# Kernel optimization log

Hardware: AMD Instinct MI355X
Metric: run time of the kernel (lower is better)

## Reference

```python
import jax, jax.numpy as jnp
from jax import lax
import numpy as np

# db4 filter bank (pywt convention): rec_lo is the canonical Daubechies-4 scaling filter
_REC_LO = np.array([0.23037781330885523, 0.7148465705525415, 0.6308807679295904,
                    -0.02798376941698385, -0.18703481171888114, 0.030841381835986965,
                    0.032883011666982945, -0.010597401784997278])
L = 8
_DEC_LO = _REC_LO[::-1].copy()
_DEC_HI = _REC_LO * ((-1.0) ** (np.arange(L) + 1))  # pywt dec_hi
_REC_HI = _DEC_HI[::-1].copy()
LEVEL = 2


def dwt_step(x):
    """Single-level DWT, pywt 'symmetric' mode. x: (N, S) -> a, d: (N, floor((S+L-1)/2))."""
    n, s = x.shape
    ext = jnp.pad(x, ((0, 0), (L - 1, L - 1)), mode='symmetric')[:, 1:]  # start at conv index 1
    # XLA conv is correlation; flip dec filters to get true convolution
    k = jnp.stack([_DEC_LO[::-1], _DEC_HI[::-1]]).astype(x.dtype)[:, None, :]  # (2,1,L)
    y = lax.conv_general_dilated(ext[:, None, :], k, window_strides=(2,), padding='VALID',
                                 dimension_numbers=('NCH', 'OIH', 'NCH'))  # (N,2,Lc)
    return y[:, 0], y[:, 1]


def idwt_step(a, d):
    """Single-level inverse DWT (pywt). Output length 2*la - L + 2."""
    la = a.shape[1]
    coef = jnp.stack([a, d], axis=1)  # (N,2,la)
    k = jnp.stack([_REC_LO[::-1], _REC_HI[::-1]]).astype(a.dtype)[None, :, :]  # (1,2,L) summed over a/d
    y = lax.conv_general_dilated(coef, k, window_strides=(1,), padding=[(L - 1, L - 1)],
                                 lhs_dilation=(2,),  # upsample-by-2 then full convolution
                                 dimension_numbers=('NCH', 'OIH', 'NCH'))  # (N,1,2la+L-2)
    return y[:, 0, L - 2: L - 2 + (2 * la - L + 2)]


def soft(c, t):
    return jnp.sign(c) * jnp.maximum(jnp.abs(c) - t, 0.0)


def denoise_2d(x2d):
    """x2d: (N, S) batch of signals; wavedec->soft-threshold->waverec, per-signal threshold."""
    s = x2d.shape[1]
    a = x2d
    details = []  # appended finest-first: [d1, d2]
    for _ in range(LEVEL):
        a, d = dwt_step(a)
        details.append(d)
    d1 = details[0]  # coeffs[-1] in pywt ordering = finest detail
    sigma = jnp.median(jnp.abs(d1), axis=1) / 0.6745
    thr = (sigma * jnp.sqrt(2.0 * jnp.log(jnp.asarray(s, x2d.dtype))))[:, None]
    rec = soft(a, thr)
    for d in details[::-1]:  # coarsest-first reconstruction
        d = soft(d, thr)
        rec = rec[:, : d.shape[1]]  # pywt waverec crops approx when one longer than detail
        rec = idwt_step(rec, d)
    return rec[:, :s]


def setup_inputs() -> dict:
    key = jax.random.key(0)
    x = jax.random.normal(key, (32, 8192, 64), dtype=jnp.float32)
    return {"x": x}


def reference(x):
    b, s, f = x.shape
    x2 = jnp.transpose(x, (0, 2, 1)).reshape(b * f, s)  # (B*F, S): every signal independent
    y = denoise_2d(x2)
    return y.reshape(b, f, s).transpose(0, 2, 1)
```

## Files before the change

kernel.cpp:

```cpp
#include <hip/hip_runtime.h>

#define S0LEN 8192
#define L1LEN 4099
#define L2LEN 2053
#define NROWS 2048
#define NT    256
#define NT2   512

constexpr float DEC_LO[8] = {
  -0.010597401784997278f,  0.032883011666982945f,  0.030841381835986965f,
  -0.18703481171888114f,  -0.02798376941698385f,   0.6308807679295904f,
   0.7148465705525415f,    0.23037781330885523f };
constexpr float DEC_HI[8] = {
  -0.23037781330885523f,   0.7148465705525415f,   -0.6308807679295904f,
  -0.02798376941698385f,   0.18703481171888114f,   0.030841381835986965f,
  -0.032883011666982945f, -0.010597401784997278f };
constexpr float REC_LO[8] = {
   0.23037781330885523f,   0.7148465705525415f,    0.6308807679295904f,
  -0.02798376941698385f,  -0.18703481171888114f,   0.030841381835986965f,
   0.032883011666982945f, -0.010597401784997278f };
constexpr float REC_HI[8] = {
  -0.010597401784997278f, -0.032883011666982945f,  0.030841381835986965f,
   0.18703481171888114f,  -0.02798376941698385f,  -0.6308807679295904f,
   0.7148465705525415f,   -0.23037781330885523f };

__device__ __forceinline__ int refl(int m, int n) {
  m = (m < 0) ? (-1 - m) : m;
  m = (m >= n) ? (2 * n - 1 - m) : m;
  return m;
}

__device__ __forceinline__ float softf(float c, float t) {
  float m = fmaxf(fabsf(c) - t, 0.0f);
  return copysignf(m, c);
}

__device__ __forceinline__ void dwt_stage(const float* __restrict__ src, int n_in,
                                          float* __restrict__ outA,
                                          float* __restrict__ outD,
                                          int n_out, int t) {
  const float2* s2 = reinterpret_cast<const float2*>(src);
  const int ihi = (n_in - 2) >> 1;
  for (int i = t; i < n_out; i += NT2) {
    float f[8];
    if (i >= 3 && i <= ihi) {
      const float2 v0 = s2[i - 3], v1 = s2[i - 2], v2 = s2[i - 1], v3 = s2[i];
      f[0] = v0.x; f[1] = v0.y; f[2] = v1.x; f[3] = v1.y;
      f[4] = v2.x; f[5] = v2.y; f[6] = v3.x; f[7] = v3.y;
    } else {
      const int base = 2 * i - 6;
#pragma unroll
      for (int q = 0; q < 8; ++q) f[q] = src[refl(base + q, n_in)];
    }
    float aa = 0.0f, dd = 0.0f;
#pragma unroll
    for (int q = 0; q < 8; ++q) {
      aa = fmaf(DEC_LO[7 - q], f[q], aa);
      dd = fmaf(DEC_HI[7 - q], f[q], dd);
    }
    outA[i] = aa;
    outD[i] = dd;
  }
}

__global__ void __launch_bounds__(NT)
k_transpose_fwd(const float* __restrict__ x, float* __restrict__ xt) {
  const int b  = blockIdx.y;
  const int s0 = blockIdx.x * 64;
  __shared__ float tile[64][65];
  const int t = threadIdx.x;
  const float* xb = x + (size_t)b * S0LEN * 64;

  const int c4 = t & 15;
  const int sl = t >> 4;
#pragma unroll
  for (int k = 0; k < 4; ++k) {
    const int s = sl + 16 * k;
    const float4 v = *reinterpret_cast<const float4*>(xb + (size_t)(s0 + s) * 64 + 4 * c4);
    tile[s][4 * c4 + 0] = v.x; tile[s][4 * c4 + 1] = v.y;
    tile[s][4 * c4 + 2] = v.z; tile[s][4 * c4 + 3] = v.w;
  }
  __syncthreads();

  const int m = t & 15;
  const int f = t >> 4;
#pragma unroll
  for (int k = 0; k < 4; ++k) {
    const int ff = f + 16 * k;
    float4 v;
    v.x = tile[4 * m + 0][ff]; v.y = tile[4 * m + 1][ff];
    v.z = tile[4 * m + 2][ff]; v.w = tile[4 * m + 3][ff];
    *reinterpret_cast<float4*>(xt + (size_t)(b * 64 + ff) * S0LEN + s0 + 4 * m) = v;
  }
}

__global__ void __launch_bounds__(NT2)
k_denoise(float* __restrict__ ws) {
  const int r = blockIdx.x;
  float* row = ws + (size_t)r * S0LEN;

  __shared__ alignas(16) float sA[8208];
  __shared__ alignas(16) float sa1[4100];
  __shared__ alignas(16) float sd1[4100];
  __shared__ unsigned histp[8 * 256];
  __shared__ unsigned wsum[4];
  __shared__ int sh_bin, sh_k;
  const int t = threadIdx.x;

  {
    const float4* src4 = reinterpret_cast<const float4*>(row);
    float4* dst4 = reinterpret_cast<float4*>(sA);
    for (int k = t; k < S0LEN / 4; k += NT2) dst4[k] = src4[k];
  }
  __syncthreads();

  dwt_stage(sA, S0LEN, sa1, sd1, L1LEN, t);
  __syncthreads();

  dwt_stage(sa1, L1LEN, sA, sA + L2LEN, L2LEN, t);
  __syncthreads();

  unsigned* ud = reinterpret_cast<unsigned*>(sA + 2 * L2LEN);
  unsigned prefval = 0u, himask = 0u;
  int k = 2049;
#pragma unroll
  for (int pass = 0; pass < 4; ++pass) {
    const int shift = 24 - 8 * pass;
    for (int i = t; i < 8 * 256; i += NT2) histp[i] = 0u;
    __syncthreads();
    unsigned* myh = histp + (t >> 6) * 256;
    if (pass == 0) {
      for (int i = t; i < L1LEN; i += NT2) {
        const unsigned u = __float_as_uint(fabsf(sd1[i]));
        ud[i] = u;
        atomicAdd(&myh[u >> 24], 1u);
      }
    } else {
      for (int i = t; i < L1LEN; i += NT2) {
        const unsigned u = ud[i];
        if ((u & himask) == prefval) atomicAdd(&myh[(u >> shift) & 255u], 1u);
      }
    }
    __syncthreads();
    unsigned c = 0u, incl = 0u;
    if (t < 256) {
#pragma unroll
      for (int w = 0; w < 8; ++w) c += histp[w * 256 + t];
      incl = c;
#pragma unroll
      for (int d = 1; d < 64; d <<= 1) {
        const unsigned n = __shfl_up(incl, d, 64);
        if ((t & 63) >= d) incl += n;
      }
      if ((t & 63) == 63) wsum[t >> 6] = incl;
    }
    __syncthreads();
    if (t < 256) {
      unsigned base = 0u;
      for (int w = 0; w < (t >> 6); ++w) base += wsum[w];
      incl += base;
      if ((unsigned)k < incl && (unsigned)k >= incl - c) {
        sh_bin = t; sh_k = k - (int)(incl - c);
      }
    }
    __syncthreads();
    prefval |= ((unsigned)sh_bin) << shift;
    himask  |= 255u << shift;
    k = sh_k;
  }
  const float median = __uint_as_float(prefval);
  const float thr = (median / 0.6745f) * sqrtf(2.0f * logf(8192.0f));

  for (int i = t; i < 2 * L2LEN; i += NT2) sA[i] = softf(sA[i], thr);
  for (int i = t; i < L1LEN; i += NT2)     sd1[i] = softf(sd1[i], thr);
  __syncthreads();

  {
    const float* a2 = sA;
    const float* d2 = sA + L2LEN;
    float* rec1 = sA + 2 * L2LEN;
    for (int p = t; p <= 2049; p += NT2) {
      float av[4], dv[4];
#pragma unroll
      for (int c2 = 0; c2 < 4; ++c2) { av[c2] = a2[p + c2]; dv[c2] = d2[p + c2]; }
      float e = 0.0f, o = 0.0f;
#pragma unroll
      for (int u = 0; u < 4; ++u) {
        e = fmaf(av[3 - u], REC_LO[2 * u],     e);
        e = fmaf(dv[3 - u], REC_HI[2 * u],     e);
        o = fmaf(av[3 - u], REC_LO[2 * u + 1], o);
        o = fmaf(dv[3 - u], REC_HI[2 * u + 1], o);
      }
      rec1[2 * p] = e;
      if (2 * p + 1 < L1LEN) rec1[2 * p + 1] = o;
    }
  }
  __syncthreads();

  {
    const float* rec1 = sA + 2 * L2LEN;
    for (int q = t; q < S0LEN / 4; q += NT2) {
      float ra[5], rd[5];
#pragma unroll
      for (int c2 = 0; c2 < 5; ++c2) { ra[c2] = rec1[2 * q + c2]; rd[c2] = sd1[2 * q + c2]; }
      float4 v;
      float acc;
      acc = 0.0f;
#pragma unroll
      for (int u = 0; u < 4; ++u) {
        acc = fmaf(ra[3 - u], REC_LO[2 * u], acc);
        acc = fmaf(rd[3 - u], REC_HI[2 * u], acc);
      }
      v.x = acc;
      acc = 0.0f;
#pragma unroll
      for (int u = 0; u < 4; ++u) {
        acc = fmaf(ra[3 - u], REC_LO[2 * u + 1], acc);
        acc = fmaf(rd[3 - u], REC_HI[2 * u + 1], acc);
      }
      v.y = acc;
      acc = 0.0f;
#pragma unroll
      for (int u = 0; u < 4; ++u) {
        acc = fmaf(ra[4 - u], REC_LO[2 * u], acc);
        acc = fmaf(rd[4 - u], REC_HI[2 * u], acc);
      }
      v.z = acc;
      acc = 0.0f;
#pragma unroll
      for (int u = 0; u < 4; ++u) {
        acc = fmaf(ra[4 - u], REC_LO[2 * u + 1], acc);
        acc = fmaf(rd[4 - u], REC_HI[2 * u + 1], acc);
      }
      v.w = acc;
      reinterpret_cast<float4*>(row)[q] = v;
    }
  }
}

__global__ void __launch_bounds__(NT)
k_transpose_bwd(const float* __restrict__ xt, float* __restrict__ out) {
  const int b  = blockIdx.y;
  const int s0 = blockIdx.x * 64;
  __shared__ float tile[64][65];
  const int t = threadIdx.x;

  const int m = t & 15;
  const int f = t >> 4;
#pragma unroll
  for (int k = 0; k < 4; ++k) {
    const int ff = f + 16 * k;
    const float4 v = *reinterpret_cast<const float4*>(xt + (size_t)(b * 64 + ff) * S0LEN + s0 + 4 * m);
    tile[ff][4 * m + 0] = v.x; tile[ff][4 * m + 1] = v.y;
    tile[ff][4 * m + 2] = v.z; tile[ff][4 * m + 3] = v.w;
  }
  __syncthreads();

  float* ob = out + (size_t)b * S0LEN * 64;
  const int c4 = t & 15;
  const int sl = t >> 4;
#pragma unroll
  for (int k = 0; k < 4; ++k) {
    const int s = sl + 16 * k;
    float4 v;
    v.x = tile[4 * c4 + 0][s]; v.y = tile[4 * c4 + 1][s];
    v.z = tile[4 * c4 + 2][s]; v.w = tile[4 * c4 + 3][s];
    *reinterpret_cast<float4*>(ob + (size_t)(s0 + s) * 64 + 4 * c4) = v;
  }
}

extern "C" void kernel_launch(void* const* d_in, const int* in_sizes, int n_in,
                              void* d_out, int out_size, void* d_ws, size_t ws_size,
                              hipStream_t stream) {
  (void)in_sizes; (void)n_in; (void)out_size; (void)ws_size;
  const float* x = (const float*)d_in[0];
  float* out = (float*)d_out;
  float* ws  = (float*)d_ws;

  const dim3 gT(S0LEN / 64, 32);

  hipLaunchKernelGGL(k_transpose_fwd, gT, dim3(NT), 0, stream, x, ws);
  hipLaunchKernelGGL(k_denoise, dim3(NROWS), dim3(NT2), 0, stream, ws);
  hipLaunchKernelGGL(k_transpose_bwd, gT, dim3(NT), 0, stream, ws, out);
}
```

Before: 194.9 us.

## Rework transposes with swizzled tiles and shrink denoise LDS footprint

Both transpose kernels now move 256-sample tiles with 512 threads, using an XOR swizzle in place of padding so shared-memory reads and writes can be full float4. The denoise kernel loads the signal in two halves into a smaller buffer so the block uses much less LDS, and adds a launch-bounds occupancy hint. Each thread computes pairs of DWT outputs from vectorised loads, the soft-threshold is fused into the inverse transform instead of a separate pass, and the histogram is reduced to four copies. These changes aim to raise occupancy and cut LDS traffic and barriers, at the cost of more complex boundary handling and an extra global reload of the row.

```diff
diff --git a/kernel.cpp b/kernel.cpp
--- a/kernel.cpp
+++ b/kernel.cpp
@@ -4,7 +4,7 @@
 #define L1LEN 4099
 #define L2LEN 2053
 #define NROWS 2048
-#define NT    256
+#define NTT   512
 #define NT2   512
 
 constexpr float DEC_LO[8] = {
@@ -35,122 +35,175 @@
   return copysignf(m, c);
 }
 
-__device__ __forceinline__ void dwt_stage(const float* __restrict__ src, int n_in,
-                                          float* __restrict__ outA,
-                                          float* __restrict__ outD,
-                                          int n_out, int t) {
-  const float2* s2 = reinterpret_cast<const float2*>(src);
-  const int ihi = (n_in - 2) >> 1;
-  for (int i = t; i < n_out; i += NT2) {
-    float f[8];
-    if (i >= 3 && i <= ihi) {
-      const float2 v0 = s2[i - 3], v1 = s2[i - 2], v2 = s2[i - 1], v3 = s2[i];
-      f[0] = v0.x; f[1] = v0.y; f[2] = v1.x; f[3] = v1.y;
-      f[4] = v2.x; f[5] = v2.y; f[6] = v3.x; f[7] = v3.y;
-    } else {
-      const int base = 2 * i - 6;
-#pragma unroll
-      for (int q = 0; q < 8; ++q) f[q] = src[refl(base + q, n_in)];
-    }
-    float aa = 0.0f, dd = 0.0f;
-#pragma unroll
-    for (int q = 0; q < 8; ++q) {
-      aa = fmaf(DEC_LO[7 - q], f[q], aa);
-      dd = fmaf(DEC_HI[7 - q], f[q], dd);
-    }
-    outA[i] = aa;
-    outD[i] = dd;
-  }
-}
-
-__global__ void __launch_bounds__(NT)
+__device__ __forceinline__ void dwt_pair_vec(const float* __restrict__ buf,
+                                             int e2, int e4a, int e4b,
+                                             float& ae, float& de, float& ao, float& dd) {
+  const float2 w01 = reinterpret_cast<const float2*>(buf)[e2];
+  const float4 w25 = reinterpret_cast<const float4*>(buf)[e4a];
+  const float4 w69 = reinterpret_cast<const float4*>(buf)[e4b];
+  const float w[10] = {w01.x, w01.y, w25.x, w25.y, w25.z, w25.w,
+                       w69.x, w69.y, w69.z, w69.w};
+  ae = de = ao = dd = 0.f;
+#pragma unroll
+  for (int q = 0; q < 8; ++q) {
+    ae = fmaf(DEC_LO[7 - q], w[q],     ae);
+    de = fmaf(DEC_HI[7 - q], w[q],     de);
+    ao = fmaf(DEC_LO[7 - q], w[q + 2], ao);
+    dd = fmaf(DEC_HI[7 - q], w[q + 2], dd);
+  }
+}
+
+__device__ __forceinline__ void dwt_scalar(const float* __restrict__ buf, int gbase,
+                                           int i, int n, float& a, float& d) {
+  a = d = 0.f;
+#pragma unroll
+  for (int q = 0; q < 8; ++q) {
+    const float v = buf[refl(2 * i - 6 + q, n) - gbase];
+    a = fmaf(DEC_LO[7 - q], v, a);
+    d = fmaf(DEC_HI[7 - q], v, d);
+  }
+}
+
+__device__ __forceinline__ float4 idwt_quad(const float* __restrict__ w,
+                                            const float* __restrict__ v) {
+  float4 o; float acc;
+  acc = 0.f;
+#pragma unroll
+  for (int u = 0; u < 4; ++u) { acc = fmaf(w[3-u], REC_LO[2*u],   acc); acc = fmaf(v[3-u], REC_HI[2*u],   acc); }
+  o.x = acc;
+  acc = 0.f;
+#pragma unroll
+  for (int u = 0; u < 4; ++u) { acc = fmaf(w[3-u], REC_LO[2*u+1], acc); acc = fmaf(v[3-u], REC_HI[2*u+1], acc); }
+  o.y = acc;
+  acc = 0.f;
+#pragma unroll
+  for (int u = 0; u < 4; ++u) { acc = fmaf(w[4-u], REC_LO[2*u],   acc); acc = fmaf(v[4-u], REC_HI[2*u],   acc); }
+  o.z = acc;
+  acc = 0.f;
+#pragma unroll
+  for (int u = 0; u < 4; ++u) { acc = fmaf(w[4-u], REC_LO[2*u+1], acc); acc = fmaf(v[4-u], REC_HI[2*u+1], acc); }
+  o.w = acc;
+  return o;
+}
+
+__global__ void __launch_bounds__(NTT)
 k_transpose_fwd(const float* __restrict__ x, float* __restrict__ xt) {
   const int b  = blockIdx.y;
-  const int s0 = blockIdx.x * 64;
-  __shared__ float tile[64][65];
+  const int s0 = blockIdx.x * 256;
+  __shared__ float tile[64][256];
   const int t = threadIdx.x;
-  const float* xb = x + (size_t)b * S0LEN * 64;
-
-  const int c4 = t & 15;
-  const int sl = t >> 4;
-#pragma unroll
-  for (int k = 0; k < 4; ++k) {
-    const int s = sl + 16 * k;
-    const float4 v = *reinterpret_cast<const float4*>(xb + (size_t)(s0 + s) * 64 + 4 * c4);
-    tile[s][4 * c4 + 0] = v.x; tile[s][4 * c4 + 1] = v.y;
-    tile[s][4 * c4 + 2] = v.z; tile[s][4 * c4 + 3] = v.w;
-  }
-  __syncthreads();
-
-  const int m = t & 15;
-  const int f = t >> 4;
-#pragma unroll
-  for (int k = 0; k < 4; ++k) {
-    const int ff = f + 16 * k;
-    float4 v;
-    v.x = tile[4 * m + 0][ff]; v.y = tile[4 * m + 1][ff];
-    v.z = tile[4 * m + 2][ff]; v.w = tile[4 * m + 3][ff];
-    *reinterpret_cast<float4*>(xt + (size_t)(b * 64 + ff) * S0LEN + s0 + 4 * m) = v;
-  }
-}
-
-__global__ void __launch_bounds__(NT2)
+  const int lane = t & 63;
+  const int wv = t >> 6;
+
+  const float* src = x + ((size_t)b * S0LEN + s0) * 64;
+  float4 rg[8];
+#pragma unroll
+  for (int k = 0; k < 8; ++k)
+    rg[k] = reinterpret_cast<const float4*>(src)[t + NTT * k];
+#pragma unroll
+  for (int k = 0; k < 8; ++k) {
+    const int n  = t + NTT * k;
+    const int s  = n >> 4;
+    const int fg = n & 15;
+    const int sc = s ^ (4 * (fg & 7));
+    tile[4 * fg + 0][sc] = rg[k].x;
+    tile[4 * fg + 1][sc] = rg[k].y;
+    tile[4 * fg + 2][sc] = rg[k].z;
+    tile[4 * fg + 3][sc] = rg[k].w;
+  }
+  __syncthreads();
+#pragma unroll
+  for (int j = 0; j < 8; ++j) {
+    const int f = 8 * wv + j;
+    const int swz = 4 * ((f >> 2) & 7);
+    const float4 v = *reinterpret_cast<const float4*>(&tile[f][(4 * lane) ^ swz]);
+    reinterpret_cast<float4*>(xt + (size_t)(b * 64 + f) * S0LEN + s0)[lane] = v;
+  }
+}
+
+__global__ void __launch_bounds__(NT2, 6)
 k_denoise(float* __restrict__ ws) {
   const int r = blockIdx.x;
   float* row = ws + (size_t)r * S0LEN;
 
-  __shared__ alignas(16) float sA[8208];
-  __shared__ alignas(16) float sa1[4100];
-  __shared__ alignas(16) float sd1[4100];
-  __shared__ unsigned histp[8 * 256];
+  __shared__ alignas(16) float X[4112];
+  __shared__ alignas(16) float A[4100];
+  __shared__ alignas(16) float D[4100];
+  __shared__ unsigned hist[1024];
   __shared__ unsigned wsum[4];
   __shared__ int sh_bin, sh_k;
   const int t = threadIdx.x;
 
   {
-    const float4* src4 = reinterpret_cast<const float4*>(row);
-    float4* dst4 = reinterpret_cast<float4*>(sA);
-    for (int k = t; k < S0LEN / 4; k += NT2) dst4[k] = src4[k];
-  }
-  __syncthreads();
-
-  dwt_stage(sA, S0LEN, sa1, sd1, L1LEN, t);
-  __syncthreads();
-
-  dwt_stage(sa1, L1LEN, sA, sA + L2LEN, L2LEN, t);
-  __syncthreads();
-
-  unsigned* ud = reinterpret_cast<unsigned*>(sA + 2 * L2LEN);
+    const float4* s4 = reinterpret_cast<const float4*>(row);
+    float4* d4 = reinterpret_cast<float4*>(X);
+    for (int j = t; j < 1027; j += NT2) d4[j] = s4[j];
+  }
+  __syncthreads();
+
+  for (int p = t; p < 1024; p += NT2) {
+    float ae, de, ao, dd;
+    if (p >= 2) dwt_pair_vec(X, 2 * p - 3, p - 1, p, ae, de, ao, dd);
+    else { dwt_scalar(X, 0, 2 * p, S0LEN, ae, de); dwt_scalar(X, 0, 2 * p + 1, S0LEN, ao, dd); }
+    reinterpret_cast<float2*>(A)[p] = make_float2(ae, ao);
+    reinterpret_cast<float2*>(D)[p] = make_float2(de, dd);
+  }
+  __syncthreads();
+
+  {
+    const float4* s4 = reinterpret_cast<const float4*>(row) + 1022;
+    float4* d4 = reinterpret_cast<float4*>(X);
+    for (int j = t; j < 1026; j += NT2) d4[j] = s4[j];
+  }
+  __syncthreads();
+
+  for (int p0 = t; p0 < 1025; p0 += NT2) {
+    const int p = 1024 + p0;
+    float ae, de, ao, dd;
+    if (p < 2048) dwt_pair_vec(X, 2 * p - 2047, p - 1023, p - 1022, ae, de, ao, dd);
+    else { dwt_scalar(X, 4088, 2 * p, S0LEN, ae, de); dwt_scalar(X, 4088, 2 * p + 1, S0LEN, ao, dd); }
+    reinterpret_cast<float2*>(A)[p] = make_float2(ae, ao);
+    reinterpret_cast<float2*>(D)[p] = make_float2(de, dd);
+  }
+  if (t == 0) {
+    float a, d; dwt_scalar(X, 4088, 4098, S0LEN, a, d);
+    A[4098] = a; D[4098] = d;
+  }
+  __syncthreads();
+
+  for (int p = t; p < 1026; p += NT2) {
+    float ae, de, ao, dd;
+    if (p >= 2 && p <= 1023) dwt_pair_vec(A, 2 * p - 3, p - 1, p, ae, de, ao, dd);
+    else { dwt_scalar(A, 0, 2 * p, L1LEN, ae, de); dwt_scalar(A, 0, 2 * p + 1, L1LEN, ao, dd); }
+    reinterpret_cast<float2*>(X)[p] = make_float2(ae, ao);
+    reinterpret_cast<float2*>(X)[1028 + p] = make_float2(de, dd);
+  }
+  if (t == 1) {
+    float a, d; dwt_scalar(A, 0, 2052, L1LEN, a, d);
+    X[2052] = a; X[2056 + 2052] = d;
+  }
+  __syncthreads();
+
   unsigned prefval = 0u, himask = 0u;
-  int k = 2049;
-#pragma unroll
+  int kk = 2049;
   for (int pass = 0; pass < 4; ++pass) {
     const int shift = 24 - 8 * pass;
-    for (int i = t; i < 8 * 256; i += NT2) histp[i] = 0u;
+    for (int i = t; i < 1024; i += NT2) hist[i] = 0u;
     __syncthreads();
-    unsigned* myh = histp + (t >> 6) * 256;
-    if (pass == 0) {
-      for (int i = t; i < L1LEN; i += NT2) {
-        const unsigned u = __float_as_uint(fabsf(sd1[i]));
-        ud[i] = u;
-        atomicAdd(&myh[u >> 24], 1u);
-      }
-    } else {
-      for (int i = t; i < L1LEN; i += NT2) {
-        const unsigned u = ud[i];
-        if ((u & himask) == prefval) atomicAdd(&myh[(u >> shift) & 255u], 1u);
-      }
+    unsigned* myh = hist + ((t >> 7) << 8);
+    for (int i = t; i < L1LEN; i += NT2) {
+      const unsigned u = __float_as_uint(fabsf(D[i]));
+      if ((u & himask) == prefval) atomicAdd(&myh[(u >> shift) & 255u], 1u);
     }
     __syncthreads();
     unsigned c = 0u, incl = 0u;
     if (t < 256) {
-#pragma unroll
-      for (int w = 0; w < 8; ++w) c += histp[w * 256 + t];
+      c = hist[t] + hist[t + 256] + hist[t + 512] + hist[t + 768];
       incl = c;
 #pragma unroll
-      for (int d = 1; d < 64; d <<= 1) {
-        const unsigned n = __shfl_up(incl, d, 64);
-        if ((t & 63) >= d) incl += n;
+      for (int dlt = 1; dlt < 64; dlt <<= 1) {
+        const unsigned nn = __shfl_up(incl, dlt, 64);
+        if ((t & 63) >= dlt) incl += nn;
       }
       if ((t & 63) == 63) wsum[t >> 6] = incl;
     }
@@ -159,113 +212,91 @@
       unsigned base = 0u;
       for (int w = 0; w < (t >> 6); ++w) base += wsum[w];
       incl += base;
-      if ((unsigned)k < incl && (unsigned)k >= incl - c) {
-        sh_bin = t; sh_k = k - (int)(incl - c);
+      if ((unsigned)kk < incl && (unsigned)kk >= incl - c) {
+        sh_bin = t; sh_k = kk - (int)(incl - c);
       }
     }
     __syncthreads();
     prefval |= ((unsigned)sh_bin) << shift;
     himask  |= 255u << shift;
-    k = sh_k;
-  }
-  const float median = __uint_as_float(prefval);
-  const float thr = (median / 0.6745f) * sqrtf(2.0f * logf(8192.0f));
-
-  for (int i = t; i < 2 * L2LEN; i += NT2) sA[i] = softf(sA[i], thr);
-  for (int i = t; i < L1LEN; i += NT2)     sd1[i] = softf(sd1[i], thr);
-  __syncthreads();
+    kk = sh_k;
+  }
+  const float thr = (__uint_as_float(prefval) / 0.6745f) * sqrtf(2.0f * logf(8192.0f));
 
   {
-    const float* a2 = sA;
-    const float* d2 = sA + L2LEN;
-    float* rec1 = sA + 2 * L2LEN;
-    for (int p = t; p <= 2049; p += NT2) {
-      float av[4], dv[4];
-#pragma unroll
-      for (int c2 = 0; c2 < 4; ++c2) { av[c2] = a2[p + c2]; dv[c2] = d2[p + c2]; }
-      float e = 0.0f, o = 0.0f;
+    const float* a2 = X;
+    const float* d2 = X + 2056;
+    for (int q = t; q < 1024; q += NT2) {
+      const float2 a0 = reinterpret_cast<const float2*>(a2)[q];
+      const float2 a1 = reinterpret_cast<const float2*>(a2)[q + 1];
+      const float  a4 = a2[2 * q + 4];
+      const float2 b0 = reinterpret_cast<const float2*>(d2)[q];
+      const float2 b1 = reinterpret_cast<const float2*>(d2)[q + 1];
+      const float  b4 = d2[2 * q + 4];
+      const float w[5] = {softf(a0.x, thr), softf(a0.y, thr), softf(a1.x, thr),
+                          softf(a1.y, thr), softf(a4, thr)};
+      const float v[5] = {softf(b0.x, thr), softf(b0.y, thr), softf(b1.x, thr),
+                          softf(b1.y, thr), softf(b4, thr)};
+      reinterpret_cast<float4*>(A)[q] = idwt_quad(w, v);
+    }
+    if (t < 3) {
+      const int i = 4096 + t, p = i >> 1, oo = i & 1;
+      float acc = 0.f;
 #pragma unroll
       for (int u = 0; u < 4; ++u) {
-        e = fmaf(av[3 - u], REC_LO[2 * u],     e);
-        e = fmaf(dv[3 - u], REC_HI[2 * u],     e);
-        o = fmaf(av[3 - u], REC_LO[2 * u + 1], o);
-        o = fmaf(dv[3 - u], REC_HI[2 * u + 1], o);
+        acc = fmaf(softf(a2[p + 3 - u], thr), REC_LO[2 * u + oo], acc);
+        acc = fmaf(softf(d2[p + 3 - u], thr), REC_HI[2 * u + oo], acc);
       }
-      rec1[2 * p] = e;
-      if (2 * p + 1 < L1LEN) rec1[2 * p + 1] = o;
-    }
-  }
-  __syncthreads();
-
-  {
-    const float* rec1 = sA + 2 * L2LEN;
-    for (int q = t; q < S0LEN / 4; q += NT2) {
-      float ra[5], rd[5];
-#pragma unroll
-      for (int c2 = 0; c2 < 5; ++c2) { ra[c2] = rec1[2 * q + c2]; rd[c2] = sd1[2 * q + c2]; }
-      float4 v;
-      float acc;
-      acc = 0.0f;
-#pragma unroll
-      for (int u = 0; u < 4; ++u) {
-        acc = fmaf(ra[3 - u], REC_LO[2 * u], acc);
-        acc = fmaf(rd[3 - u], REC_HI[2 * u], acc);
-      }
-      v.x = acc;
-      acc = 0.0f;
-#pragma unroll
-      for (int u = 0; u < 4; ++u) {
-        acc = fmaf(ra[3 - u], REC_LO[2 * u + 1], acc);
-        acc = fmaf(rd[3 - u], REC_HI[2 * u + 1], acc);
-      }
-      v.y = acc;
-      acc = 0.0f;
-#pragma unroll
-      for (int u = 0; u < 4; ++u) {
-        acc = fmaf(ra[4 - u], REC_LO[2 * u], acc);
-        acc = fmaf(rd[4 - u], REC_HI[2 * u], acc);
-      }
-      v.z = acc;
-      acc = 0.0f;
-#pragma unroll
-      for (int u = 0; u < 4; ++u) {
-        acc = fmaf(ra[4 - u], REC_LO[2 * u + 1], acc);
-        acc = fmaf(rd[4 - u], REC_HI[2 * u + 1], acc);
-      }
-      v.w = acc;
-      reinterpret_cast<float4*>(row)[q] = v;
-    }
-  }
-}
-
-__global__ void __launch_bounds__(NT)
+      A[i] = acc;
+    }
+  }
+  __syncthreads();
+
+  for (int q = t; q < 2048; q += NT2) {
+    const float2 r0 = reinterpret_cast<const float2*>(A)[q];
+    const float2 r1 = reinterpret_cast<const float2*>(A)[q + 1];
+    const float  r4 = A[2 * q + 4];
+    const float2 e0 = reinterpret_cast<const float2*>(D)[q];
+    const float2 e1 = reinterpret_cast<const float2*>(D)[q + 1];
+    const float  e4 = D[2 * q + 4];
+    const float w[5] = {r0.x, r0.y, r1.x, r1.y, r4};
+    const float v[5] = {softf(e0.x, thr), softf(e0.y, thr), softf(e1.x, thr),
+                        softf(e1.y, thr), softf(e4, thr)};
+    reinterpret_cast<float4*>(row)[q] = idwt_quad(w, v);
+  }
+}
+
+__global__ void __launch_bounds__(NTT)
 k_transpose_bwd(const float* __restrict__ xt, float* __restrict__ out) {
   const int b  = blockIdx.y;
-  const int s0 = blockIdx.x * 64;
-  __shared__ float tile[64][65];
+  const int s0 = blockIdx.x * 256;
+  __shared__ float tile[64][256];
   const int t = threadIdx.x;
-
-  const int m = t & 15;
-  const int f = t >> 4;
-#pragma unroll
-  for (int k = 0; k < 4; ++k) {
-    const int ff = f + 16 * k;
-    const float4 v = *reinterpret_cast<const float4*>(xt + (size_t)(b * 64 + ff) * S0LEN + s0 + 4 * m);
-    tile[ff][4 * m + 0] = v.x; tile[ff][4 * m + 1] = v.y;
-    tile[ff][4 * m + 2] = v.z; tile[ff][4 * m + 3] = v.w;
-  }
-  __syncthreads();
-
-  float* ob = out + (size_t)b * S0LEN * 64;
-  const int c4 = t & 15;
-  const int sl = t >> 4;
-#pragma unroll
-  for (int k = 0; k < 4; ++k) {
-    const int s = sl + 16 * k;
+  const int lane = t & 63;
+  const int wv = t >> 6;
+
+#pragma unroll
+  for (int j = 0; j < 8; ++j) {
+    const int f = 8 * wv + j;
+    const int swz = 4 * ((f >> 2) & 7);
+    const float4 v = reinterpret_cast<const float4*>(xt + (size_t)(b * 64 + f) * S0LEN + s0)[lane];
+    *reinterpret_cast<float4*>(&tile[f][(4 * lane) ^ swz]) = v;
+  }
+  __syncthreads();
+
+  float* dst = out + ((size_t)b * S0LEN + s0) * 64;
+#pragma unroll
+  for (int k = 0; k < 8; ++k) {
+    const int n  = t + NTT * k;
+    const int s  = n >> 4;
+    const int fg = n & 15;
+    const int sc = s ^ (4 * (fg & 7));
     float4 v;
-    v.x = tile[4 * c4 + 0][s]; v.y = tile[4 * c4 + 1][s];
-    v.z = tile[4 * c4 + 2][s]; v.w = tile[4 * c4 + 3][s];
-    *reinterpret_cast<float4*>(ob + (size_t)(s0 + s) * 64 + 4 * c4) = v;
+    v.x = tile[4 * fg + 0][sc];
+    v.y = tile[4 * fg + 1][sc];
+    v.z = tile[4 * fg + 2][sc];
+    v.w = tile[4 * fg + 3][sc];
+    reinterpret_cast<float4*>(dst)[n] = v;
   }
 }
 
@@ -277,9 +308,8 @@
   float* out = (float*)d_out;
   float* ws  = (float*)d_ws;
 
-  const dim3 gT(S0LEN / 64, 32);
-
-  hipLaunchKernelGGL(k_transpose_fwd, gT, dim3(NT), 0, stream, x, ws);
+  const dim3 gT(S0LEN / 256, 32);
+  hipLaunchKernelGGL(k_transpose_fwd, gT, dim3(NTT), 0, stream, x, ws);
   hipLaunchKernelGGL(k_denoise, dim3(NROWS), dim3(NT2), 0, stream, ws);
-  hipLaunchKernelGGL(k_transpose_bwd, gT, dim3(NT), 0, stream, ws, out);
-}
+  hipLaunchKernelGGL(k_transpose_bwd, gT, dim3(NTT), 0, stream, ws, out);
+}
```

Measured after the change: 189.3 us. -2.8%, faster.
